# Kernel tuning notes

Measured on AMD Instinct MI355X. Metric: run time of the kernel, lower is better.

Reference implementation:

```python
import math
import jax, jax.numpy as jnp
import numpy as np

EMBED = 512
FF = 1024
NG = 50
RBF_RADIUS = 12.0
NUM_ELEMENTS = 100
B = 64        # graphs per batch
NPG = 64      # atoms per graph
N = B * NPG   # 4096 atoms
K = 32        # fixed in/out degree per atom
E = N * K     # 131072 edges
INV_SQRT2 = 1.0 / math.sqrt(2.0)


def gaussian_smearing(d, start, stop, ng):
    offset = jnp.linspace(start, stop, ng)
    coeff = -0.5 / (offset[1] - offset[0]) ** 2
    return jnp.exp(coeff * (d[..., None] - offset) ** 2)


def setup_inputs() -> dict:
    key = jax.random.key(0)
    ks = jax.random.split(key, 8)
    pos = jax.random.normal(ks[0], (N, 3), dtype=jnp.float32) * 5.0
    natoms = jnp.full((B,), NPG, dtype=jnp.int32)
    atomic_numbers = jax.random.randint(ks[1], (N,), 1, NUM_ELEMENTS).astype(jnp.int32)
    # structured edge_index: node with local index l connects to (l+1..l+K) mod NPG
    # -> every node has exactly K outgoing and K incoming edges (static dnd/sns sizes)
    base = np.arange(NPG)
    src_local = np.repeat(base, K)
    dst_local = (src_local + np.tile(np.arange(1, K + 1), NPG)) % NPG
    offs = (np.arange(B) * NPG)[:, None]
    src = (offs + src_local[None, :]).reshape(-1)
    dst = (offs + dst_local[None, :]).reshape(-1)
    edge_index = jnp.asarray(np.stack([src, dst]), dtype=jnp.int32)
    # learned params
    emb_table = jax.random.normal(ks[2], (NUM_ELEMENTS, EMBED), dtype=jnp.float32) * 0.02
    emb_table = emb_table.at[0].set(0.0)  # padding_idx=0
    type_embedding = jax.random.normal(ks[3], (2, 1, EMBED), dtype=jnp.float32)
    w1 = jax.random.normal(ks[4], (NG, FF), dtype=jnp.float32) / math.sqrt(NG)
    b1 = jnp.zeros((FF,), dtype=jnp.float32)
    w2 = jax.random.normal(ks[5], (FF, EMBED), dtype=jnp.float32) / math.sqrt(FF)
    b2 = jnp.zeros((EMBED,), dtype=jnp.float32)
    return {"pos": pos, "natoms": natoms, "atomic_numbers": atomic_numbers,
            "edge_index": edge_index, "emb_table": emb_table,
            "type_embedding": type_embedding, "w1": w1, "b1": b1, "w2": w2, "b2": b2}


def reference(pos, natoms, atomic_numbers, edge_index, emb_table, type_embedding, w1, b1, w2, b2):
    n_nodes = pos.shape[0]
    n_edges = edge_index.shape[1]
    n_graphs = natoms.shape[0]
    npg = n_nodes // n_graphs          # equal-size graphs (matches setup_inputs)
    k = n_edges // n_nodes             # fixed degree

    # ---- node tokens ----
    atom_emb = emb_table[atomic_numbers]                       # [N, D]
    tok_nodes = INV_SQRT2 * (atom_emb + type_embedding[0])

    # ---- edge tokens ----
    src, dst = edge_index[0], edge_index[1]
    vec = pos[dst] - pos[src]                                   # [E, 3]
    dist = jnp.linalg.norm(vec, axis=-1)                        # [E]
    vec_hat = vec / jnp.maximum(dist, 1e-12)[:, None]           # F.normalize
    rbfs = gaussian_smearing(dist, 0.0, RBF_RADIUS, NG)         # [E, NG]
    h = jax.nn.silu(rbfs @ w1 + b1)                             # ResMLP hidden [E, FF]
    edge_feat = h @ w2 + b2                                     # [E, D]
    tok_edges = INV_SQRT2 * (edge_feat + type_embedding[1])
    tokens = jnp.concatenate([tok_nodes, tok_edges], axis=0)    # [N+E, D]

    # ---- intra-graph fully connected edges (vectorized over equal-size graphs) ----
    ar = jnp.arange(npg, dtype=edge_index.dtype)
    within = jnp.stack([jnp.tile(ar, npg), jnp.repeat(ar, npg)], axis=0)  # [2, npg^2]
    offs = jnp.arange(n_graphs, dtype=edge_index.dtype) * npg
    all_edges = (within[:, None, :] + offs[None, :, None]).reshape(2, -1)  # [2, B*npg^2]
    all_vec = pos[all_edges[1]] - pos[all_edges[0]]
    all_dist = jnp.linalg.norm(all_vec, axis=-1)

    # ---- node<->edge-token connectivity ----
    etp = n_nodes + jnp.arange(n_edges, dtype=edge_index.dtype)  # edge token ids
    n2e = jnp.stack([src, etp], axis=0)
    e2n = jnp.stack([etp, dst], axis=0)

    # edge pairs sharing a node (equivalent of the scipy CSR products),
    # exploiting fixed degree k for static shapes. Output is sorted by row
    # then column, matching CSR coo ordering.
    def shared_node_pairs(node_ids):
        order = jnp.argsort(node_ids)            # stable: ascending edge ids per node
        groups = order.reshape(n_nodes, k)       # [N, k] edge ids grouped by node
        rows = jnp.repeat(jnp.arange(n_edges, dtype=edge_index.dtype), k)
        cols = groups[node_ids].reshape(-1).astype(edge_index.dtype)
        return jnp.stack([rows, cols], axis=0) + n_nodes  # [2, E*k]

    dnd = shared_node_pairs(dst)  # e2n @ e2n.T : edges sharing a destination node
    sns = shared_node_pairs(src)  # n2e.T @ n2e : edges sharing a source node

    edges = jnp.concatenate([all_edges, n2e, e2n, dnd, sns], axis=1)

    cosine_dd = jnp.sum(vec_hat[dnd[0] - n_nodes] * vec_hat[dnd[1] - n_nodes], axis=1)
    cosine_ss = jnp.sum(vec_hat[sns[0] - n_nodes] * vec_hat[sns[1] - n_nodes], axis=1)

    return (tokens, edges, vec_hat, all_dist, dist, cosine_dd, cosine_ss)
```

## Files before the change

### kernel.cpp

```cpp
#include <hip/hip_runtime.h>
#include <math.h>

constexpr int N_  = 4096;
constexpr int E_  = 131072;
constexpr int D_  = 512;
constexpr int FF_ = 1024;
constexpr int NG_ = 50;
constexpr int K_  = 32;
constexpr float INV_SQRT2 = 0.70710678118654752440f;
constexpr float RBF_DELTA = 12.0f / 49.0f;
constexpr float RBF_COEFF = -0.5f * (49.0f/12.0f) * (49.0f/12.0f);

constexpr long long TE_COLS  = 262144LL + 131072 + 131072 + 4194304 + 4194304;
constexpr long long OFF_TOK   = 0;
constexpr long long OFF_EDGES = (long long)(N_ + E_) * D_;
constexpr long long OFF_VHAT  = OFF_EDGES + 2 * TE_COLS;
constexpr long long OFF_ADIST = OFF_VHAT + (long long)E_ * 3;
constexpr long long OFF_DIST  = OFF_ADIST + 262144;
constexpr long long OFF_CDD   = OFF_DIST + E_;
constexpr long long OFF_CSS   = OFF_CDD + (long long)E_ * K_;
constexpr long long EC_ALL = 0;
constexpr long long EC_N2E = 262144;
constexpr long long EC_E2N = 393216;
constexpr long long EC_DND = 524288;
constexpr long long EC_SNS = 4718592;

typedef __attribute__((ext_vector_type(8))) short   short8;
typedef __attribute__((ext_vector_type(4))) short   s16x4;
typedef __attribute__((ext_vector_type(8))) __bf16  bf16x8;
typedef __attribute__((ext_vector_type(4))) float   f32x4;

static __device__ inline short f2bf(float x) {
    unsigned u = __float_as_uint(x);
    u = (u + 0x7FFFu + ((u >> 16) & 1u)) >> 16;
    return (short)u;
}
static __device__ inline f32x4 MFMA(short8 a, short8 b, f32x4 c) {
    return __builtin_amdgcn_mfma_f32_16x16x32_bf16(
        __builtin_bit_cast(bf16x8, a), __builtin_bit_cast(bf16x8, b), c, 0, 0, 0);
}

__global__ void k_node_tokens(const int* __restrict__ an, const float* __restrict__ emb,
                              const float* __restrict__ te, float* __restrict__ out)
{
    int idx = blockIdx.x * 256 + threadIdx.x;
    int n  = idx >> 7;
    int c  = (idx & 127) << 2;
    float4 e4 = *(const float4*)&emb[(size_t)an[n] * D_ + c];
    float4 t4 = *(const float4*)&te[c];
    float4 r;
    r.x = INV_SQRT2 * (e4.x + t4.x);
    r.y = INV_SQRT2 * (e4.y + t4.y);
    r.z = INV_SQRT2 * (e4.z + t4.z);
    r.w = INV_SQRT2 * (e4.w + t4.w);
    *(float4*)&out[OFF_TOK + (size_t)n * D_ + c] = r;
}

__global__ void k_edge_geom(const float* __restrict__ pos, const int* __restrict__ ei,
                            float* __restrict__ out, int* __restrict__ cntD,
                            int* __restrict__ cntS, int* __restrict__ gD,
                            int* __restrict__ gS)
{
    int e = blockIdx.x * 256 + threadIdx.x;
    int s = ei[e];
    int d = ei[E_ + e];
    float vx = pos[3*d+0] - pos[3*s+0];
    float vy = pos[3*d+1] - pos[3*s+1];
    float vz = pos[3*d+2] - pos[3*s+2];
    float dist = sqrtf(vx*vx + vy*vy + vz*vz);
    out[OFF_DIST + e] = dist;
    float inv = 1.0f / fmaxf(dist, 1e-12f);
    out[OFF_VHAT + (size_t)e*3 + 0] = vx * inv;
    out[OFF_VHAT + (size_t)e*3 + 1] = vy * inv;
    out[OFF_VHAT + (size_t)e*3 + 2] = vz * inv;
    out[OFF_EDGES + EC_N2E + e]           = (float)s;
    out[OFF_EDGES + TE_COLS + EC_N2E + e] = (float)(N_ + e);
    out[OFF_EDGES + EC_E2N + e]           = (float)(N_ + e);
    out[OFF_EDGES + TE_COLS + EC_E2N + e] = (float)d;
    int rd = atomicAdd(&cntD[d], 1);
    gD[(size_t)d * K_ + rd] = e;
    int rs = atomicAdd(&cntS[s], 1);
    gS[(size_t)s * K_ + rs] = e;
}

__global__ void k_all_pairs(const float* __restrict__ pos, float* __restrict__ out)
{
    int c = blockIdx.x * 256 + threadIdx.x;
    int b = c >> 12;
    int p = c & 4095;
    int i0 = b * 64 + (p & 63);
    int i1 = b * 64 + (p >> 6);
    out[OFF_EDGES + EC_ALL + c]           = (float)i0;
    out[OFF_EDGES + TE_COLS + EC_ALL + c] = (float)i1;
    float dx = pos[3*i1+0] - pos[3*i0+0];
    float dy = pos[3*i1+1] - pos[3*i0+1];
    float dz = pos[3*i1+2] - pos[3*i0+2];
    out[OFF_ADIST + c] = sqrtf(dx*dx + dy*dy + dz*dz);
}

__global__ void k_sort_groups(int* __restrict__ groups)
{
    int gid = blockIdx.x * 256 + threadIdx.x;
    if (gid >= 2 * N_) return;
    int* p = groups + (size_t)gid * K_;
    int v[32];
    #pragma unroll
    for (int i = 0; i < 32; ++i) v[i] = p[i];
    #pragma unroll
    for (int k = 2; k <= 32; k <<= 1) {
        #pragma unroll
        for (int j = k >> 1; j > 0; j >>= 1) {
            #pragma unroll
            for (int i = 0; i < 32; ++i) {
                int l = i ^ j;
                if (l > i) {
                    int a = v[i], b = v[l];
                    bool sw = ((i & k) == 0) ? (a > b) : (a < b);
                    v[i] = sw ? b : a;
                    v[l] = sw ? a : b;
                }
            }
        }
    }
    #pragma unroll
    for (int i = 0; i < 32; ++i) p[i] = v[i];
}

__global__ void k_dnd_sns(const int* __restrict__ ei, const int* __restrict__ gD,
                          const int* __restrict__ gS, float* __restrict__ out)
{
    int idx = blockIdx.x * 256 + threadIdx.x;
    int e  = idx >> 3;
    int j0 = (idx & 7) * 4;
    int s  = ei[e];
    int d  = ei[E_ + e];
    const float* vh = out + OFF_VHAT;
    float hx = vh[(size_t)e*3+0], hy = vh[(size_t)e*3+1], hz = vh[(size_t)e*3+2];
    size_t ib = (size_t)e * K_ + j0;
    float4 rowv;
    rowv.x = rowv.y = rowv.z = rowv.w = (float)(N_ + e);

    int4 g1 = *(const int4*)&gD[(size_t)d * K_ + j0];
    float4 c1, x1;
    c1.x = (float)(N_ + g1.x); c1.y = (float)(N_ + g1.y);
    c1.z = (float)(N_ + g1.z); c1.w = (float)(N_ + g1.w);
    x1.x = hx*vh[(size_t)g1.x*3+0] + hy*vh[(size_t)g1.x*3+1] + hz*vh[(size_t)g1.x*3+2];
    x1.y = hx*vh[(size_t)g1.y*3+0] + hy*vh[(size_t)g1.y*3+1] + hz*vh[(size_t)g1.y*3+2];
    x1.z = hx*vh[(size_t)g1.z*3+0] + hy*vh[(size_t)g1.z*3+1] + hz*vh[(size_t)g1.z*3+2];
    x1.w = hx*vh[(size_t)g1.w*3+0] + hy*vh[(size_t)g1.w*3+1] + hz*vh[(size_t)g1.w*3+2];
    *(float4*)&out[OFF_EDGES + EC_DND + ib]           = rowv;
    *(float4*)&out[OFF_EDGES + TE_COLS + EC_DND + ib] = c1;
    *(float4*)&out[OFF_CDD + ib]                      = x1;

    int4 g2 = *(const int4*)&gS[(size_t)s * K_ + j0];
    float4 c2, x2;
    c2.x = (float)(N_ + g2.x); c2.y = (float)(N_ + g2.y);
    c2.z = (float)(N_ + g2.z); c2.w = (float)(N_ + g2.w);
    x2.x = hx*vh[(size_t)g2.x*3+0] + hy*vh[(size_t)g2.x*3+1] + hz*vh[(size_t)g2.x*3+2];
    x2.y = hx*vh[(size_t)g2.y*3+0] + hy*vh[(size_t)g2.y*3+1] + hz*vh[(size_t)g2.y*3+2];
    x2.z = hx*vh[(size_t)g2.z*3+0] + hy*vh[(size_t)g2.z*3+1] + hz*vh[(size_t)g2.z*3+2];
    x2.w = hx*vh[(size_t)g2.w*3+0] + hy*vh[(size_t)g2.w*3+1] + hz*vh[(size_t)g2.w*3+2];
    *(float4*)&out[OFF_EDGES + EC_SNS + ib]           = rowv;
    *(float4*)&out[OFF_EDGES + TE_COLS + EC_SNS + ib] = c2;
    *(float4*)&out[OFF_CSS + ib]                      = x2;
}

__global__ void k_prep_w(const float* __restrict__ w1, const float* __restrict__ w2,
                         short* __restrict__ w1f, short* __restrict__ w2f)
{
    int idx = blockIdx.x * 256 + threadIdx.x;
    if (idx < 65536) {
        int i = idx & 7, L = (idx >> 3) & 63, kblk = (idx >> 9) & 1, cb = idx >> 10;
        int k = kblk*32 + (L >> 4)*8 + i, col = cb*16 + (L & 15);
        float v = (k < NG_) ? w1[(size_t)k * FF_ + col] : 0.0f;
        w1f[idx] = f2bf(v);
    } else {
        int j = idx - 65536;
        if (j < 524288) {
            int i = j & 7, cc = (j >> 3) & 15, kg = (j >> 7) & 3;
            int cblk = (j >> 9) & 31, kblk = j >> 14;
            int k = kblk*32 + kg*8 + i, col = cblk*16 + cc;
            w2f[j] = f2bf(w2[(size_t)k * D_ + col]);
        }
    }
}

__global__ __launch_bounds__(512, 4) void k_edge_fused(
    const short* __restrict__ w1f, const short* __restrict__ w2f,
    const float* __restrict__ b1, const float* __restrict__ b2,
    const float* __restrict__ te, float* __restrict__ out)
{
    __shared__ short s_rbf[4096];
    __shared__ short s_h[2][4096];
    const int tid = threadIdx.x;
    const int e0  = blockIdx.x * 64;

    {
        int f = tid;
        int lane = f & 63, kblk = (f >> 6) & 1, mf = f >> 7;
        int e_local = mf*16 + (lane & 15);
        int k0 = kblk*32 + (lane >> 4) * 8;
        float dist = out[OFF_DIST + e0 + e_local];
        short8 v;
        #pragma unroll
        for (int i = 0; i < 8; ++i) {
            int k = k0 + i;
            float val = 0.0f;
            if (k < NG_) { float dd = dist - (float)k * RBF_DELTA; val = __expf(RBF_COEFF*dd*dd); }
            v[i] = f2bf(val);
        }
        *(short8*)&s_rbf[f * 8] = v;
    }
    __syncthreads();

    const int w  = tid >> 6, L = tid & 63;
    const int kg = L >> 4, lc = L & 15;
    const int ft    = w >> 1;
    const int ebase = (w & 1) * 2;

    short8 br[2][2];
    #pragma unroll
    for (int j = 0; j < 2; ++j)
        #pragma unroll
        for (int kb = 0; kb < 2; ++kb)
            br[j][kb] = *(const short8*)&s_rbf[(((ebase + j)*2 + kb)*64 + L) * 8];

    const int ffc0 = ft*16 + kg*4;
    const int skb  = ffc0 >> 5;
    const int sisl = ffc0 & 7;
    const int sl2  = ((ffc0 & 31) >> 3)*16 + lc;

    const f32x4 Z = {0.0f, 0.0f, 0.0f, 0.0f};
    f32x4 acc[4][4];
    #pragma unroll
    for (int m = 0; m < 4; ++m)
        #pragma unroll
        for (int n = 0; n < 4; ++n) acc[m][n] = Z;

    for (int c = 0; c < 16; ++c) {
        int cb = c*4 + ft;
        short8 aw0 = *(const short8*)&w1f[((cb*2 + 0)*64 + L) * 8];
        short8 aw1 = *(const short8*)&w1f[((cb*2 + 1)*64 + L) * 8];
        f32x4 b4 = *(const f32x4*)&b1[c*64 + ffc0];
        short* hb = &s_h[c & 1][0];
        #pragma unroll
        for (int j = 0; j < 2; ++j) {
            f32x4 t = MFMA(aw0, br[j][0], Z);
            f32x4 d1 = MFMA(aw1, br[j][1], t);
            s16x4 pk;
            #pragma unroll
            for (int r = 0; r < 4; ++r) {
                float x = d1[r] + b4[r];
                float sv = x * __fdividef(1.0f, 1.0f + __expf(-x));
                pk[r] = f2bf(sv);
            }
            *(s16x4*)&hb[((((ebase + j)*2 + skb)*64 + sl2) * 8) + sisl] = pk;
        }
        __syncthreads();
        const short* hr = &s_h[c & 1][0];
        #pragma unroll
        for (int kb = 0; kb < 2; ++kb) {
            short8 a2[4], bw[4];
            #pragma unroll
            for (int m = 0; m < 4; ++m)
                a2[m] = *(const short8*)&hr[((m*2 + kb)*64 + L) * 8];
            #pragma unroll
            for (int nfo = 0; nfo < 4; ++nfo)
                bw[nfo] = *(const short8*)&w2f[(((c*2 + kb)*32 + (w*4 + nfo))*64 + L) * 8];
            #pragma unroll
            for (int m = 0; m < 4; ++m)
                #pragma unroll
                for (int nfo = 0; nfo < 4; ++nfo)
                    acc[m][nfo] = MFMA(a2[m], bw[nfo], acc[m][nfo]);
        }
    }

    float bb[4];
    #pragma unroll
    for (int nfo = 0; nfo < 4; ++nfo) {
        int col = w*64 + nfo*16 + lc;
        bb[nfo] = b2[col] + te[D_ + col];
    }
    #pragma unroll
    for (int m = 0; m < 4; ++m) {
        int row0 = e0 + m*16 + kg*4;
        #pragma unroll
        for (int nfo = 0; nfo < 4; ++nfo) {
            int col = w*64 + nfo*16 + lc;
            #pragma unroll
            for (int r = 0; r < 4; ++r)
                out[OFF_TOK + (size_t)(N_ + row0 + r) * D_ + col] =
                    INV_SQRT2 * (acc[m][nfo][r] + bb[nfo]);
        }
    }
}

extern "C" void kernel_launch(void* const* d_in, const int* in_sizes, int n_in,
                              void* d_out, int out_size, void* d_ws, size_t ws_size,
                              hipStream_t stream)
{
    const float* pos = (const float*)d_in[0];
    const int*   an  = (const int*)d_in[2];
    const int*   ei  = (const int*)d_in[3];
    const float* emb = (const float*)d_in[4];
    const float* te  = (const float*)d_in[5];
    const float* w1  = (const float*)d_in[6];
    const float* b1  = (const float*)d_in[7];
    const float* w2  = (const float*)d_in[8];
    const float* b2  = (const float*)d_in[9];
    float* out = (float*)d_out;

    int* cntD = (int*)d_ws;
    int* cntS = cntD + N_;
    int* gD   = cntS + N_;
    int* gS   = gD + E_;
    short* w1f = (short*)((char*)d_ws + 1081344);
    short* w2f = w1f + 65536;

    hipMemsetAsync(cntD, 0, 2 * N_ * sizeof(int), stream);

    k_prep_w      <<<2304, 256, 0, stream>>>(w1, w2, w1f, w2f);
    k_node_tokens <<<2048, 256, 0, stream>>>(an, emb, te, out);
    k_edge_geom   <<<E_/256, 256, 0, stream>>>(pos, ei, out, cntD, cntS, gD, gS);
    k_all_pairs   <<<262144/256, 256, 0, stream>>>(pos, out);
    k_sort_groups <<<(2*N_)/256, 256, 0, stream>>>(gD);
    k_dnd_sns     <<<(E_*K_/4)/256, 256, 0, stream>>>(ei, gD, gS, out);
    k_edge_fused  <<<E_/64, 512, 0, stream>>>(w1f, w2f, b1, b2, te, out);
}
```

Measured before the change: 250.9 us.

## Merge token, all-pairs and pair-cosine kernels into the edge MLP launch

Folds node-token embedding, all-pairs distances and the dnd/sns pair-cosine writes into a single mega-kernel that dispatches on block index, alongside the MFMA edge MLP blocks. This removes three launches and lets the memory-bound write work overlap with the compute-bound MLP blocks. It also switches the bf16 conversion to the hardware cast and raises wave priority around the MFMA inner loop. The side-work blocks carry the large shared-memory footprint and launch bounds of the MLP kernel, which may limit how many of them are resident at once.

```diff
diff --git a/kernel.cpp b/kernel.cpp
--- a/kernel.cpp
+++ b/kernel.cpp
@@ -35,25 +35,12 @@
     u = (u + 0x7FFFu + ((u >> 16) & 1u)) >> 16;
     return (short)u;
 }
+static __device__ inline short f2bf_fast(float x) {
+    return __builtin_bit_cast(short, (__bf16)x);
+}
 static __device__ inline f32x4 MFMA(short8 a, short8 b, f32x4 c) {
     return __builtin_amdgcn_mfma_f32_16x16x32_bf16(
         __builtin_bit_cast(bf16x8, a), __builtin_bit_cast(bf16x8, b), c, 0, 0, 0);
-}
-
-__global__ void k_node_tokens(const int* __restrict__ an, const float* __restrict__ emb,
-                              const float* __restrict__ te, float* __restrict__ out)
-{
-    int idx = blockIdx.x * 256 + threadIdx.x;
-    int n  = idx >> 7;
-    int c  = (idx & 127) << 2;
-    float4 e4 = *(const float4*)&emb[(size_t)an[n] * D_ + c];
-    float4 t4 = *(const float4*)&te[c];
-    float4 r;
-    r.x = INV_SQRT2 * (e4.x + t4.x);
-    r.y = INV_SQRT2 * (e4.y + t4.y);
-    r.z = INV_SQRT2 * (e4.z + t4.z);
-    r.w = INV_SQRT2 * (e4.w + t4.w);
-    *(float4*)&out[OFF_TOK + (size_t)n * D_ + c] = r;
 }
 
 __global__ void k_edge_geom(const float* __restrict__ pos, const int* __restrict__ ei,
@@ -83,21 +70,6 @@
     gS[(size_t)s * K_ + rs] = e;
 }
 
-__global__ void k_all_pairs(const float* __restrict__ pos, float* __restrict__ out)
-{
-    int c = blockIdx.x * 256 + threadIdx.x;
-    int b = c >> 12;
-    int p = c & 4095;
-    int i0 = b * 64 + (p & 63);
-    int i1 = b * 64 + (p >> 6);
-    out[OFF_EDGES + EC_ALL + c]           = (float)i0;
-    out[OFF_EDGES + TE_COLS + EC_ALL + c] = (float)i1;
-    float dx = pos[3*i1+0] - pos[3*i0+0];
-    float dy = pos[3*i1+1] - pos[3*i0+1];
-    float dz = pos[3*i1+2] - pos[3*i0+2];
-    out[OFF_ADIST + c] = sqrtf(dx*dx + dy*dy + dz*dz);
-}
-
 __global__ void k_sort_groups(int* __restrict__ groups)
 {
     int gid = blockIdx.x * 256 + threadIdx.x;
@@ -124,45 +96,6 @@
     }
     #pragma unroll
     for (int i = 0; i < 32; ++i) p[i] = v[i];
-}
-
-__global__ void k_dnd_sns(const int* __restrict__ ei, const int* __restrict__ gD,
-                          const int* __restrict__ gS, float* __restrict__ out)
-{
-    int idx = blockIdx.x * 256 + threadIdx.x;
-    int e  = idx >> 3;
-    int j0 = (idx & 7) * 4;
-    int s  = ei[e];
-    int d  = ei[E_ + e];
-    const float* vh = out + OFF_VHAT;
-    float hx = vh[(size_t)e*3+0], hy = vh[(size_t)e*3+1], hz = vh[(size_t)e*3+2];
-    size_t ib = (size_t)e * K_ + j0;
-    float4 rowv;
-    rowv.x = rowv.y = rowv.z = rowv.w = (float)(N_ + e);
-
-    int4 g1 = *(const int4*)&gD[(size_t)d * K_ + j0];
-    float4 c1, x1;
-    c1.x = (float)(N_ + g1.x); c1.y = (float)(N_ + g1.y);
-    c1.z = (float)(N_ + g1.z); c1.w = (float)(N_ + g1.w);
-    x1.x = hx*vh[(size_t)g1.x*3+0] + hy*vh[(size_t)g1.x*3+1] + hz*vh[(size_t)g1.x*3+2];
-    x1.y = hx*vh[(size_t)g1.y*3+0] + hy*vh[(size_t)g1.y*3+1] + hz*vh[(size_t)g1.y*3+2];
-    x1.z = hx*vh[(size_t)g1.z*3+0] + hy*vh[(size_t)g1.z*3+1] + hz*vh[(size_t)g1.z*3+2];
-    x1.w = hx*vh[(size_t)g1.w*3+0] + hy*vh[(size_t)g1.w*3+1] + hz*vh[(size_t)g1.w*3+2];
-    *(float4*)&out[OFF_EDGES + EC_DND + ib]           = rowv;
-    *(float4*)&out[OFF_EDGES + TE_COLS + EC_DND + ib] = c1;
-    *(float4*)&out[OFF_CDD + ib]                      = x1;
-
-    int4 g2 = *(const int4*)&gS[(size_t)s * K_ + j0];
-    float4 c2, x2;
-    c2.x = (float)(N_ + g2.x); c2.y = (float)(N_ + g2.y);
-    c2.z = (float)(N_ + g2.z); c2.w = (float)(N_ + g2.w);
-    x2.x = hx*vh[(size_t)g2.x*3+0] + hy*vh[(size_t)g2.x*3+1] + hz*vh[(size_t)g2.x*3+2];
-    x2.y = hx*vh[(size_t)g2.y*3+0] + hy*vh[(size_t)g2.y*3+1] + hz*vh[(size_t)g2.y*3+2];
-    x2.z = hx*vh[(size_t)g2.z*3+0] + hy*vh[(size_t)g2.z*3+1] + hz*vh[(size_t)g2.z*3+2];
-    x2.w = hx*vh[(size_t)g2.w*3+0] + hy*vh[(size_t)g2.w*3+1] + hz*vh[(size_t)g2.w*3+2];
-    *(float4*)&out[OFF_EDGES + EC_SNS + ib]           = rowv;
-    *(float4*)&out[OFF_EDGES + TE_COLS + EC_SNS + ib] = c2;
-    *(float4*)&out[OFF_CSS + ib]                      = x2;
 }
 
 __global__ void k_prep_w(const float* __restrict__ w1, const float* __restrict__ w2,
@@ -185,15 +118,88 @@
     }
 }
 
-__global__ __launch_bounds__(512, 4) void k_edge_fused(
+__global__ __launch_bounds__(512, 4) void k_mega(
     const short* __restrict__ w1f, const short* __restrict__ w2f,
     const float* __restrict__ b1, const float* __restrict__ b2,
-    const float* __restrict__ te, float* __restrict__ out)
+    const float* __restrict__ te, const int* __restrict__ an,
+    const float* __restrict__ emb, const float* __restrict__ pos,
+    const int* __restrict__ ei, const int* __restrict__ gD,
+    const int* __restrict__ gS, float* __restrict__ out)
 {
     __shared__ short s_rbf[4096];
     __shared__ short s_h[2][4096];
+    const int bid = blockIdx.x;
     const int tid = threadIdx.x;
-    const int e0  = blockIdx.x * 64;
+
+    if (bid >= 2048) {
+        if (bid < 3072) {
+            int idx = (bid - 2048) * 512 + tid;
+            int n  = idx >> 7;
+            int c  = (idx & 127) << 2;
+            float4 e4 = *(const float4*)&emb[(size_t)an[n] * D_ + c];
+            float4 t4 = *(const float4*)&te[c];
+            float4 r;
+            r.x = INV_SQRT2 * (e4.x + t4.x);
+            r.y = INV_SQRT2 * (e4.y + t4.y);
+            r.z = INV_SQRT2 * (e4.z + t4.z);
+            r.w = INV_SQRT2 * (e4.w + t4.w);
+            *(float4*)&out[OFF_TOK + (size_t)n * D_ + c] = r;
+            return;
+        }
+        if (bid < 3584) {
+            int c = (bid - 3072) * 512 + tid;
+            int b = c >> 12;
+            int p = c & 4095;
+            int i0 = b * 64 + (p & 63);
+            int i1 = b * 64 + (p >> 6);
+            out[OFF_EDGES + EC_ALL + c]           = (float)i0;
+            out[OFF_EDGES + TE_COLS + EC_ALL + c] = (float)i1;
+            float dx = pos[3*i1+0] - pos[3*i0+0];
+            float dy = pos[3*i1+1] - pos[3*i0+1];
+            float dz = pos[3*i1+2] - pos[3*i0+2];
+            out[OFF_ADIST + c] = sqrtf(dx*dx + dy*dy + dz*dz);
+            return;
+        }
+        {
+            int idx = (bid - 3584) * 512 + tid;
+            int e  = idx >> 3;
+            int j0 = (idx & 7) * 4;
+            int s  = ei[e];
+            int d  = ei[E_ + e];
+            const float* vh = out + OFF_VHAT;
+            float hx = vh[(size_t)e*3+0], hy = vh[(size_t)e*3+1], hz = vh[(size_t)e*3+2];
+            size_t ib = (size_t)e * K_ + j0;
+            float4 rowv;
+            rowv.x = rowv.y = rowv.z = rowv.w = (float)(N_ + e);
+
+            int4 g1 = *(const int4*)&gD[(size_t)d * K_ + j0];
+            float4 c1, x1;
+            c1.x = (float)(N_ + g1.x); c1.y = (float)(N_ + g1.y);
+            c1.z = (float)(N_ + g1.z); c1.w = (float)(N_ + g1.w);
+            x1.x = hx*vh[(size_t)g1.x*3+0] + hy*vh[(size_t)g1.x*3+1] + hz*vh[(size_t)g1.x*3+2];
+            x1.y = hx*vh[(size_t)g1.y*3+0] + hy*vh[(size_t)g1.y*3+1] + hz*vh[(size_t)g1.y*3+2];
+            x1.z = hx*vh[(size_t)g1.z*3+0] + hy*vh[(size_t)g1.z*3+1] + hz*vh[(size_t)g1.z*3+2];
+            x1.w = hx*vh[(size_t)g1.w*3+0] + hy*vh[(size_t)g1.w*3+1] + hz*vh[(size_t)g1.w*3+2];
+            *(float4*)&out[OFF_EDGES + EC_DND + ib]           = rowv;
+            *(float4*)&out[OFF_EDGES + TE_COLS + EC_DND + ib] = c1;
+            *(float4*)&out[OFF_CDD + ib]                      = x1;
+
+            int4 g2 = *(const int4*)&gS[(size_t)s * K_ + j0];
+            float4 c2, x2;
+            c2.x = (float)(N_ + g2.x); c2.y = (float)(N_ + g2.y);
+            c2.z = (float)(N_ + g2.z); c2.w = (float)(N_ + g2.w);
+            x2.x = hx*vh[(size_t)g2.x*3+0] + hy*vh[(size_t)g2.x*3+1] + hz*vh[(size_t)g2.x*3+2];
+            x2.y = hx*vh[(size_t)g2.y*3+0] + hy*vh[(size_t)g2.y*3+1] + hz*vh[(size_t)g2.y*3+2];
+            x2.z = hx*vh[(size_t)g2.z*3+0] + hy*vh[(size_t)g2.z*3+1] + hz*vh[(size_t)g2.z*3+2];
+            x2.w = hx*vh[(size_t)g2.w*3+0] + hy*vh[(size_t)g2.w*3+1] + hz*vh[(size_t)g2.w*3+2];
+            *(float4*)&out[OFF_EDGES + EC_SNS + ib]           = rowv;
+            *(float4*)&out[OFF_EDGES + TE_COLS + EC_SNS + ib] = c2;
+            *(float4*)&out[OFF_CSS + ib]                      = x2;
+            return;
+        }
+    }
+
+    const int e0 = bid * 64;
 
     {
         int f = tid;
@@ -245,14 +251,14 @@
         short* hb = &s_h[c & 1][0];
         #pragma unroll
         for (int j = 0; j < 2; ++j) {
-            f32x4 t = MFMA(aw0, br[j][0], Z);
+            f32x4 t  = MFMA(aw0, br[j][0], Z);
             f32x4 d1 = MFMA(aw1, br[j][1], t);
             s16x4 pk;
             #pragma unroll
             for (int r = 0; r < 4; ++r) {
                 float x = d1[r] + b4[r];
                 float sv = x * __fdividef(1.0f, 1.0f + __expf(-x));
-                pk[r] = f2bf(sv);
+                pk[r] = f2bf_fast(sv);
             }
             *(s16x4*)&hb[((((ebase + j)*2 + skb)*64 + sl2) * 8) + sisl] = pk;
         }
@@ -267,11 +273,13 @@
             #pragma unroll
             for (int nfo = 0; nfo < 4; ++nfo)
                 bw[nfo] = *(const short8*)&w2f[(((c*2 + kb)*32 + (w*4 + nfo))*64 + L) * 8];
+            __builtin_amdgcn_s_setprio(1);
             #pragma unroll
             for (int m = 0; m < 4; ++m)
                 #pragma unroll
                 for (int nfo = 0; nfo < 4; ++nfo)
                     acc[m][nfo] = MFMA(a2[m], bw[nfo], acc[m][nfo]);
+            __builtin_amdgcn_s_setprio(0);
         }
     }
 
@@ -320,10 +328,8 @@
     hipMemsetAsync(cntD, 0, 2 * N_ * sizeof(int), stream);
 
     k_prep_w      <<<2304, 256, 0, stream>>>(w1, w2, w1f, w2f);
-    k_node_tokens <<<2048, 256, 0, stream>>>(an, emb, te, out);
     k_edge_geom   <<<E_/256, 256, 0, stream>>>(pos, ei, out, cntD, cntS, gD, gS);
-    k_all_pairs   <<<262144/256, 256, 0, stream>>>(pos, out);
     k_sort_groups <<<(2*N_)/256, 256, 0, stream>>>(gD);
-    k_dnd_sns     <<<(E_*K_/4)/256, 256, 0, stream>>>(ei, gD, gS, out);
-    k_edge_fused  <<<E_/64, 512, 0, stream>>>(w1f, w2f, b1, b2, te, out);
-}
+    k_mega        <<<5632, 512, 0, stream>>>(w1f, w2f, b1, b2, te, an, emb, pos,
+                                             ei, gD, gS, out);
+}
```

Measured after the change: 277.5 us. 10.6% more time.
